# Performance work log

Hardware: AMD Instinct MI355X
Metric: run time of the kernel (lower is better)

## Reference

```python
import jax, jax.numpy as jnp
import numpy as np

EMB = 256  # embedding_dim


def setup_inputs() -> dict:
    key = jax.random.key(0)
    k1, k2, k3 = jax.random.split(key, 3)
    B, P, N, D = 32, 4, 1024, EMB
    x = jax.random.normal(k1, (B, P, N, D), dtype=jnp.float32)
    W_qkv = jax.random.normal(k2, (D, 1 + 2 * D), dtype=jnp.float32) * (1.0 / np.sqrt(D))
    b_qkv = jnp.zeros((1 + 2 * D,), dtype=jnp.float32)
    W_o = jax.random.normal(k3, (D, D), dtype=jnp.float32) * (1.0 / np.sqrt(D))
    b_o = jnp.zeros((D,), dtype=jnp.float32)
    return {"x": x, "W_qkv": W_qkv, "b_qkv": b_qkv, "W_o": W_o, "b_o": b_o}


def reference(x, W_qkv, b_qkv, W_o, b_o):
    # x: [B, P, N, D]
    D = W_o.shape[0]
    qkv = jnp.einsum('bpnd,de->bpne', x, W_qkv) + b_qkv  # [B,P,N,1+2D]
    q = qkv[..., :1]                 # [B,P,N,1]
    k = qkv[..., 1:1 + D]            # [B,P,N,D]
    v = jax.nn.relu(qkv[..., 1 + D:])  # [B,P,N,D]
    # softmax over the patch axis N (axis=2)
    context_scores = jax.nn.softmax(q, axis=2)  # [B,P,N,1]
    # dropout layers operate in inference mode here (identity)
    context_vector = jnp.sum(k * context_scores, axis=2, keepdims=True)  # [B,P,1,D]
    updated_values = v * context_vector  # broadcast multiply, [B,P,N,D]
    final = jnp.einsum('bpnd,de->bpne', updated_values, W_o) + b_o  # [B,P,N,D]
    return final
```

## Files before the change

### kernel.cpp

```cpp
#include <hip/hip_runtime.h>


typedef float  floatx4 __attribute__((ext_vector_type(4)));
typedef __bf16 bf16x8  __attribute__((ext_vector_type(8)));
typedef unsigned short u16;
typedef u16 u16x8 __attribute__((ext_vector_type(8)));

#define NGRP 128

__device__ __forceinline__ float bf2f(u16 u) {
    union { unsigned int i; float f; } c; c.i = ((unsigned int)u) << 16; return c.f;
}
__device__ __forceinline__ u16 f2bf(float f) {
    union { __bf16 h; u16 u; } c; c.h = (__bf16)f; return c.u;
}
__device__ __forceinline__ floatx4 mfma16(bf16x8 a, bf16x8 b, floatx4 c) {
    return __builtin_amdgcn_mfma_f32_16x16x32_bf16(a, b, c, 0, 0, 0);
}

__global__ __launch_bounds__(256, 4) void k_sum(
    const float* __restrict__ x, const float* __restrict__ Wqkv,
    const float* __restrict__ Wo, const float* __restrict__ bqkv,
    float* __restrict__ y, float* __restrict__ Sg,
    u16* __restrict__ Wvp, u16* __restrict__ Wop)
{
    const int tid = threadIdx.x;
    const int m0 = blockIdx.x * 64;
    const int g  = blockIdx.x >> 4;
    const int cc = tid & 31, r0 = tid >> 5;
    const int w = tid >> 6, lane = tid & 63;
    __shared__ float e_s[64];
    __shared__ float ws4[4 * 256];

    if (blockIdx.x < 256) {
        const int i = blockIdx.x * 256 + tid;
        const int j = i & 7, pl = (i >> 3) & 63, kk = (i >> 9) & 7, ct = i >> 12;
        const int k = kk * 32 + (pl >> 4) * 8 + j;
        Wvp[i] = f2bf(Wqkv[k * 513 + (257 + ct * 16 + (pl & 15))]);
        Wop[i] = f2bf(Wo[k * 256 + (ct * 16 + (pl & 15))]);
    }

    float wqv[8];
    {
        const float* wb = Wqkv + (size_t)(cc * 8) * 513;
#pragma unroll
        for (int j = 0; j < 8; ++j) wqv[j] = wb[(size_t)j * 513];
    }

    float qp[8];
    u16x8 o[8];
#pragma unroll
    for (int i = 0; i < 8; ++i) {
        const int row = r0 + 8 * i;
        const float* xp = x + (size_t)(m0 + row) * 256 + cc * 8;
        floatx4 u0 = *(const floatx4*)xp;
        floatx4 u1 = *(const floatx4*)(xp + 4);
        qp[i] = u0[0] * wqv[0] + u0[1] * wqv[1] + u0[2] * wqv[2] + u0[3] * wqv[3]
              + u1[0] * wqv[4] + u1[1] * wqv[5] + u1[2] * wqv[6] + u1[3] * wqv[7];
        u16x8 t;
        t[0] = f2bf(u0[0]); t[1] = f2bf(u0[1]); t[2] = f2bf(u0[2]); t[3] = f2bf(u0[3]);
        t[4] = f2bf(u1[0]); t[5] = f2bf(u1[1]); t[6] = f2bf(u1[2]); t[7] = f2bf(u1[3]);
        o[i] = t;
    }

#pragma unroll
    for (int m = 1; m <= 16; m <<= 1) {
#pragma unroll
        for (int i = 0; i < 8; ++i) qp[i] += __shfl_xor(qp[i], m, 64);
    }
    if ((tid & 31) == 0) {
        const float bq0 = bqkv[0];
#pragma unroll
        for (int i = 0; i < 8; ++i) e_s[r0 + 8 * i] = __expf(qp[i] + bq0);
    }
    __syncthreads();

    float yacc[8];
#pragma unroll
    for (int j = 0; j < 8; ++j) yacc[j] = 0.f;
#pragma unroll
    for (int i = 0; i < 8; ++i) {
        const float e = e_s[r0 + 8 * i];
#pragma unroll
        for (int j = 0; j < 8; ++j) yacc[j] += e * bf2f(o[i][j]);
    }
#pragma unroll
    for (int j = 0; j < 8; ++j) yacc[j] += __shfl_xor(yacc[j], 32, 64);
    if (lane < 32) {
#pragma unroll
        for (int j = 0; j < 8; ++j) ws4[w * 256 + lane * 8 + j] = yacc[j];
    }
    __syncthreads();

    if (tid < 64) {
        float e = e_s[tid];
#pragma unroll
        for (int s = 32; s > 0; s >>= 1) e += __shfl_xor(e, s, 64);
        if (tid == 0) atomicAdd(Sg + g, e);
    }
    {
        const float s = ws4[tid] + ws4[256 + tid] + ws4[512 + tid] + ws4[768 + tid];
        atomicAdd(y + g * 256 + tid, s);
    }
}

__global__ __launch_bounds__(256) void k_cv(
    const float* __restrict__ Wqkv, const float* __restrict__ bqkv,
    const float* __restrict__ y, const float* __restrict__ Sg,
    float* __restrict__ cv)
{
    const int g = blockIdx.x, d = threadIdx.x;
    __shared__ float ys[256];
    ys[d] = y[g * 256 + d] * (1.0f / Sg[g]);
    __syncthreads();
    float acc = bqkv[1 + d];
    const float* wp = Wqkv + 1 + d;
#pragma unroll 4
    for (int t = 0; t < 256; t++) acc += ys[t] * wp[(size_t)t * 513];
    cv[g * 256 + d] = acc;
}

__global__ __launch_bounds__(256, 4) void k_vo(
    const float* __restrict__ x, const u16* __restrict__ Wvp,
    const u16* __restrict__ Wop, const float* __restrict__ cv,
    const float* __restrict__ bqkv, const float* __restrict__ bo,
    float* __restrict__ out)
{
    const int tid = threadIdx.x;
    const int w = tid >> 6, lane = tid & 63, quad = lane >> 4, n16 = lane & 15;
    const int m0 = blockIdx.x * 64;
    const int g  = blockIdx.x >> 4;
    const int cc = tid & 31, r0 = tid >> 5;

    __shared__ u16 As[64 * 256];
    __shared__ float cvs[256];

    cvs[tid] = cv[g * 256 + tid];

#pragma unroll
    for (int i = 0; i < 8; ++i) {
        const int row = r0 + 8 * i;
        const float* xp = x + (size_t)(m0 + row) * 256 + cc * 8;
        floatx4 u0 = *(const floatx4*)xp;
        floatx4 u1 = *(const floatx4*)(xp + 4);
        u16x8 t;
        t[0] = f2bf(u0[0]); t[1] = f2bf(u0[1]); t[2] = f2bf(u0[2]); t[3] = f2bf(u0[3]);
        t[4] = f2bf(u1[0]); t[5] = f2bf(u1[1]); t[6] = f2bf(u1[2]); t[7] = f2bf(u1[3]);
        *(u16x8*)(As + row * 256 + ((cc ^ (row & 15)) * 8)) = t;
    }
    __syncthreads();

    floatx4 acc[4][4];
#pragma unroll
    for (int i = 0; i < 4; i++)
#pragma unroll
        for (int rt = 0; rt < 4; rt++) acc[i][rt] = (floatx4){0.f, 0.f, 0.f, 0.f};
#pragma unroll
    for (int kk = 0; kk < 8; kk++) {
        bf16x8 a[4];
#pragma unroll
        for (int rt = 0; rt < 4; rt++) {
            const int row = rt * 16 + n16;
            a[rt] = __builtin_bit_cast(bf16x8,
                *(const u16x8*)(&As[row * 256 + (((kk * 4 + quad) ^ n16) * 8)]));
        }
#pragma unroll
        for (int i = 0; i < 4; i++) {
            const int ct = w + 4 * i;
            bf16x8 bfr = __builtin_bit_cast(bf16x8,
                *(const u16x8*)(Wvp + (size_t)((ct * 8 + kk) * 64 + lane) * 8));
#pragma unroll
            for (int rt = 0; rt < 4; rt++) acc[i][rt] = mfma16(a[rt], bfr, acc[i][rt]);
        }
    }
    __syncthreads();

#pragma unroll
    for (int i = 0; i < 4; i++) {
        const int col = (w + 4 * i) * 16 + n16;
        const float bias = bqkv[257 + col];
        const float scale = cvs[col];
        const int cchunk = col >> 3, co = col & 7;
#pragma unroll
        for (int rt = 0; rt < 4; rt++) {
#pragma unroll
            for (int r = 0; r < 4; r++) {
                const int row = rt * 16 + quad * 4 + r;
                As[row * 256 + ((cchunk ^ (row & 15)) * 8) + co] =
                    f2bf(fmaxf(acc[i][rt][r] + bias, 0.f) * scale);
            }
        }
    }
    __syncthreads();

    floatx4 acc2[4][4];
#pragma unroll
    for (int i = 0; i < 4; i++)
#pragma unroll
        for (int rt = 0; rt < 4; rt++) acc2[i][rt] = (floatx4){0.f, 0.f, 0.f, 0.f};
#pragma unroll
    for (int kk = 0; kk < 8; kk++) {
        bf16x8 a[4];
#pragma unroll
        for (int rt = 0; rt < 4; rt++) {
            const int row = rt * 16 + n16;
            a[rt] = __builtin_bit_cast(bf16x8,
                *(const u16x8*)(&As[row * 256 + (((kk * 4 + quad) ^ n16) * 8)]));
        }
#pragma unroll
        for (int i = 0; i < 4; i++) {
            const int ct = w + 4 * i;
            bf16x8 bfr = __builtin_bit_cast(bf16x8,
                *(const u16x8*)(Wop + (size_t)((ct * 8 + kk) * 64 + lane) * 8));
#pragma unroll
            for (int rt = 0; rt < 4; rt++) acc2[i][rt] = mfma16(a[rt], bfr, acc2[i][rt]);
        }
    }

#pragma unroll
    for (int i = 0; i < 4; i++) {
        const int col = (w + 4 * i) * 16 + n16;
        const float bias = bo[col];
#pragma unroll
        for (int rt = 0; rt < 4; rt++) {
            const int rowb = m0 + rt * 16 + quad * 4;
#pragma unroll
            for (int r = 0; r < 4; r++)
                out[(size_t)(rowb + r) * 256 + col] = acc2[i][rt][r] + bias;
        }
    }
}

extern "C" void kernel_launch(void* const* d_in, const int* in_sizes, int n_in,
                              void* d_out, int out_size, void* d_ws, size_t ws_size,
                              hipStream_t stream)
{
    const float* x    = (const float*)d_in[0];
    const float* Wqkv = (const float*)d_in[1];
    const float* bqkv = (const float*)d_in[2];
    const float* Wo   = (const float*)d_in[3];
    const float* bo   = (const float*)d_in[4];
    float* out = (float*)d_out;

    char* ws = (char*)d_ws;
    u16*   Wvp = (u16*)(ws);
    u16*   Wop = (u16*)(ws + 131072);
    float* cv  = (float*)(ws + 262144);
    float* y   = (float*)(ws + 393216);
    float* Sg  = (float*)(ws + 524288);

    hipMemsetAsync(ws + 393216, 0, 131584, stream);
    k_sum<<<2048, 256, 0, stream>>>(x, Wqkv, Wo, bqkv, y, Sg, Wvp, Wop);
    k_cv <<<NGRP, 256, 0, stream>>>(Wqkv, bqkv, y, Sg, cv);
    k_vo <<<2048, 256, 0, stream>>>(x, Wvp, Wop, cv, bqkv, bo, out);
}
```

Before: 339.7 us.

## Cache bf16 copy of x in k_sum, load via LDS DMA in k_vo

The first pass now writes a pre-swizzled bf16 copy of x to workspace, so the second kernel reads half the bytes and copies it straight into LDS with global_load_lds instead of re-reading fp32 x and converting it. k_vo is restructured so each wave owns 16 rows and all 16 column tiles, which removes block-level syncthreads. k_sum is reorganized into 128-row blocks with a butterfly reduction for q. The cost is an extra 64MB bf16 write in k_sum and per-wave reloads of the weight fragments from global memory.

```diff
diff --git a/kernel.cpp b/kernel.cpp
--- a/kernel.cpp
+++ b/kernel.cpp
@@ -5,6 +5,7 @@
 typedef __bf16 bf16x8  __attribute__((ext_vector_type(8)));
 typedef unsigned short u16;
 typedef u16 u16x8 __attribute__((ext_vector_type(8)));
+typedef u16 u16x4 __attribute__((ext_vector_type(4)));
 
 #define NGRP 128
 
@@ -16,92 +17,105 @@
 }
 __device__ __forceinline__ floatx4 mfma16(bf16x8 a, bf16x8 b, floatx4 c) {
     return __builtin_amdgcn_mfma_f32_16x16x32_bf16(a, b, c, 0, 0, 0);
+}
+
+__device__ __forceinline__ void dma16(const u16* src, u16* lds) {
+    __builtin_amdgcn_global_load_lds(
+        (const __attribute__((address_space(1))) unsigned int*)src,
+        (__attribute__((address_space(3))) unsigned int*)lds, 16, 0, 0);
 }
 
 __global__ __launch_bounds__(256, 4) void k_sum(
     const float* __restrict__ x, const float* __restrict__ Wqkv,
     const float* __restrict__ Wo, const float* __restrict__ bqkv,
     float* __restrict__ y, float* __restrict__ Sg,
-    u16* __restrict__ Wvp, u16* __restrict__ Wop)
+    u16* __restrict__ xb, u16* __restrict__ Wvp, u16* __restrict__ Wop)
 {
     const int tid = threadIdx.x;
-    const int m0 = blockIdx.x * 64;
-    const int g  = blockIdx.x >> 4;
-    const int cc = tid & 31, r0 = tid >> 5;
     const int w = tid >> 6, lane = tid & 63;
-    __shared__ float e_s[64];
-    __shared__ float ws4[4 * 256];
-
-    if (blockIdx.x < 256) {
-        const int i = blockIdx.x * 256 + tid;
+    const int b = blockIdx.x;
+    const int g = b >> 3;
+
+    __shared__ float e_s[4][16];
+
+    if (b < 256) {
+        const int i = b * 256 + tid;
         const int j = i & 7, pl = (i >> 3) & 63, kk = (i >> 9) & 7, ct = i >> 12;
         const int k = kk * 32 + (pl >> 4) * 8 + j;
         Wvp[i] = f2bf(Wqkv[k * 513 + (257 + ct * 16 + (pl & 15))]);
         Wop[i] = f2bf(Wo[k * 256 + (ct * 16 + (pl & 15))]);
     }
 
-    float wqv[8];
-    {
-        const float* wb = Wqkv + (size_t)(cc * 8) * 513;
-#pragma unroll
-        for (int j = 0; j < 8; ++j) wqv[j] = wb[(size_t)j * 513];
-    }
-
-    float qp[8];
-    u16x8 o[8];
-#pragma unroll
-    for (int i = 0; i < 8; ++i) {
-        const int row = r0 + 8 * i;
-        const float* xp = x + (size_t)(m0 + row) * 256 + cc * 8;
-        floatx4 u0 = *(const floatx4*)xp;
-        floatx4 u1 = *(const floatx4*)(xp + 4);
-        qp[i] = u0[0] * wqv[0] + u0[1] * wqv[1] + u0[2] * wqv[2] + u0[3] * wqv[3]
-              + u1[0] * wqv[4] + u1[1] * wqv[5] + u1[2] * wqv[6] + u1[3] * wqv[7];
-        u16x8 t;
-        t[0] = f2bf(u0[0]); t[1] = f2bf(u0[1]); t[2] = f2bf(u0[2]); t[3] = f2bf(u0[3]);
-        t[4] = f2bf(u1[0]); t[5] = f2bf(u1[1]); t[6] = f2bf(u1[2]); t[7] = f2bf(u1[3]);
-        o[i] = t;
-    }
-
-#pragma unroll
-    for (int m = 1; m <= 16; m <<= 1) {
-#pragma unroll
-        for (int i = 0; i < 8; ++i) qp[i] += __shfl_xor(qp[i], m, 64);
-    }
-    if ((tid & 31) == 0) {
-        const float bq0 = bqkv[0];
-#pragma unroll
-        for (int i = 0; i < 8; ++i) e_s[r0 + 8 * i] = __expf(qp[i] + bq0);
-    }
-    __syncthreads();
-
-    float yacc[8];
-#pragma unroll
-    for (int j = 0; j < 8; ++j) yacc[j] = 0.f;
-#pragma unroll
-    for (int i = 0; i < 8; ++i) {
-        const float e = e_s[r0 + 8 * i];
-#pragma unroll
-        for (int j = 0; j < 8; ++j) yacc[j] += e * bf2f(o[i][j]);
-    }
-#pragma unroll
-    for (int j = 0; j < 8; ++j) yacc[j] += __shfl_xor(yacc[j], 32, 64);
-    if (lane < 32) {
-#pragma unroll
-        for (int j = 0; j < 8; ++j) ws4[w * 256 + lane * 8 + j] = yacc[j];
-    }
-    __syncthreads();
-
-    if (tid < 64) {
-        float e = e_s[tid];
-#pragma unroll
-        for (int s = 32; s > 0; s >>= 1) e += __shfl_xor(e, s, 64);
-        if (tid == 0) atomicAdd(Sg + g, e);
-    }
-    {
-        const float s = ws4[tid] + ws4[256 + tid] + ws4[512 + tid] + ws4[768 + tid];
-        atomicAdd(y + g * 256 + tid, s);
-    }
+    const float bq0 = bqkv[0];
+
+    float wqv[4];
+#pragma unroll
+    for (int c = 0; c < 4; ++c) wqv[c] = Wqkv[(size_t)(lane * 4 + c) * 513];
+
+    float yacc[4] = {0.f, 0.f, 0.f, 0.f};
+    float Sacc = 0.f;
+
+#pragma unroll
+    for (int s = 0; s < 2; ++s) {
+        const int m0 = b * 128 + w * 16 + s * 64;
+        u16* xt = xb + (size_t)(b * 8 + w + s * 4) * 4096;
+
+        float p[16];
+        u16x4 o[16];
+#pragma unroll
+        for (int r = 0; r < 16; ++r) {
+            floatx4 u = *(const floatx4*)(x + (size_t)(m0 + r) * 256 + lane * 4);
+            p[r] = u[0] * wqv[0] + u[1] * wqv[1] + u[2] * wqv[2] + u[3] * wqv[3];
+            u16x4 h;
+            h[0] = f2bf(u[0]); h[1] = f2bf(u[1]); h[2] = f2bf(u[2]); h[3] = f2bf(u[3]);
+            o[r] = h;
+            *(u16x4*)(xt + r * 256 + (((lane >> 1) ^ r) * 8 + (lane & 1) * 4)) = h;
+        }
+
+        float t8[8];
+#pragma unroll
+        for (int i = 0; i < 8; ++i) {
+            const float a = p[2 * i], c = p[2 * i + 1];
+            t8[i] = ((lane & 1) ? c : a) + __shfl_xor((lane & 1) ? a : c, 1, 64);
+        }
+        float t4[4];
+#pragma unroll
+        for (int i = 0; i < 4; ++i) {
+            const float a = t8[2 * i], c = t8[2 * i + 1];
+            t4[i] = ((lane & 2) ? c : a) + __shfl_xor((lane & 2) ? a : c, 2, 64);
+        }
+        float t2[2];
+#pragma unroll
+        for (int i = 0; i < 2; ++i) {
+            const float a = t4[2 * i], c = t4[2 * i + 1];
+            t2[i] = ((lane & 4) ? c : a) + __shfl_xor((lane & 4) ? a : c, 4, 64);
+        }
+        float q;
+        {
+            const float a = t2[0], c = t2[1];
+            q = ((lane & 8) ? c : a) + __shfl_xor((lane & 8) ? a : c, 8, 64);
+        }
+        q += __shfl_xor(q, 16, 64);
+        q += __shfl_xor(q, 32, 64);
+
+        const float e = __expf(q + bq0);
+        if (lane < 16) { e_s[w][lane] = e; Sacc += e; }
+
+#pragma unroll
+        for (int r = 0; r < 16; ++r) {
+            const float er = e_s[w][r];
+            yacc[0] += er * bf2f(o[r][0]);
+            yacc[1] += er * bf2f(o[r][1]);
+            yacc[2] += er * bf2f(o[r][2]);
+            yacc[3] += er * bf2f(o[r][3]);
+        }
+    }
+
+#pragma unroll
+    for (int m = 1; m <= 32; m <<= 1) Sacc += __shfl_xor(Sacc, m, 64);
+    if (lane == 0) atomicAdd(Sg + g, Sacc);
+#pragma unroll
+    for (int j = 0; j < 4; ++j) atomicAdd(y + g * 256 + lane * 4 + j, yacc[j]);
 }
 
 __global__ __launch_bounds__(256) void k_cv(
@@ -121,113 +135,81 @@
 }
 
 __global__ __launch_bounds__(256, 4) void k_vo(
-    const float* __restrict__ x, const u16* __restrict__ Wvp,
+    const u16* __restrict__ xb, const u16* __restrict__ Wvp,
     const u16* __restrict__ Wop, const float* __restrict__ cv,
     const float* __restrict__ bqkv, const float* __restrict__ bo,
     float* __restrict__ out)
 {
     const int tid = threadIdx.x;
-    const int w = tid >> 6, lane = tid & 63, quad = lane >> 4, n16 = lane & 15;
-    const int m0 = blockIdx.x * 64;
-    const int g  = blockIdx.x >> 4;
-    const int cc = tid & 31, r0 = tid >> 5;
-
-    __shared__ u16 As[64 * 256];
-    __shared__ float cvs[256];
-
-    cvs[tid] = cv[g * 256 + tid];
-
-#pragma unroll
-    for (int i = 0; i < 8; ++i) {
-        const int row = r0 + 8 * i;
-        const float* xp = x + (size_t)(m0 + row) * 256 + cc * 8;
-        floatx4 u0 = *(const floatx4*)xp;
-        floatx4 u1 = *(const floatx4*)(xp + 4);
-        u16x8 t;
-        t[0] = f2bf(u0[0]); t[1] = f2bf(u0[1]); t[2] = f2bf(u0[2]); t[3] = f2bf(u0[3]);
-        t[4] = f2bf(u1[0]); t[5] = f2bf(u1[1]); t[6] = f2bf(u1[2]); t[7] = f2bf(u1[3]);
-        *(u16x8*)(As + row * 256 + ((cc ^ (row & 15)) * 8)) = t;
-    }
-    __syncthreads();
-
-    floatx4 acc[4][4];
-#pragma unroll
-    for (int i = 0; i < 4; i++)
-#pragma unroll
-        for (int rt = 0; rt < 4; rt++) acc[i][rt] = (floatx4){0.f, 0.f, 0.f, 0.f};
-#pragma unroll
-    for (int kk = 0; kk < 8; kk++) {
-        bf16x8 a[4];
-#pragma unroll
-        for (int rt = 0; rt < 4; rt++) {
-            const int row = rt * 16 + n16;
-            a[rt] = __builtin_bit_cast(bf16x8,
-                *(const u16x8*)(&As[row * 256 + (((kk * 4 + quad) ^ n16) * 8)]));
-        }
-#pragma unroll
-        for (int i = 0; i < 4; i++) {
-            const int ct = w + 4 * i;
+    const int w = tid >> 6, lane = tid & 63;
+    const int quad = lane >> 4, n16 = lane & 15;
+    const int j = blockIdx.x * 4 + w;
+    const int m0 = j * 16;
+    const int g  = j >> 6;
+
+    __shared__ u16 As[4][4096];
+    u16* S = As[w];
+
+    {
+        const u16* src = xb + (size_t)j * 4096;
+#pragma unroll
+        for (int i = 0; i < 8; ++i)
+            dma16(src + i * 512 + lane * 8, S + i * 512);
+    }
+    __builtin_amdgcn_sched_barrier(0);
+    asm volatile("s_waitcnt vmcnt(0)" ::: "memory");
+    __builtin_amdgcn_sched_barrier(0);
+
+    floatx4 acc[16];
+#pragma unroll
+    for (int ct = 0; ct < 16; ++ct) acc[ct] = (floatx4){0.f, 0.f, 0.f, 0.f};
+#pragma unroll
+    for (int kk = 0; kk < 8; ++kk) {
+        bf16x8 a = __builtin_bit_cast(bf16x8,
+            *(const u16x8*)(S + n16 * 256 + (((kk * 4 + quad) ^ n16) * 8)));
+#pragma unroll
+        for (int ct = 0; ct < 16; ++ct) {
             bf16x8 bfr = __builtin_bit_cast(bf16x8,
                 *(const u16x8*)(Wvp + (size_t)((ct * 8 + kk) * 64 + lane) * 8));
-#pragma unroll
-            for (int rt = 0; rt < 4; rt++) acc[i][rt] = mfma16(a[rt], bfr, acc[i][rt]);
-        }
-    }
-    __syncthreads();
-
-#pragma unroll
-    for (int i = 0; i < 4; i++) {
-        const int col = (w + 4 * i) * 16 + n16;
-        const float bias = bqkv[257 + col];
-        const float scale = cvs[col];
-        const int cchunk = col >> 3, co = col & 7;
-#pragma unroll
-        for (int rt = 0; rt < 4; rt++) {
-#pragma unroll
-            for (int r = 0; r < 4; r++) {
-                const int row = rt * 16 + quad * 4 + r;
-                As[row * 256 + ((cchunk ^ (row & 15)) * 8) + co] =
-                    f2bf(fmaxf(acc[i][rt][r] + bias, 0.f) * scale);
-            }
-        }
-    }
-    __syncthreads();
-
-    floatx4 acc2[4][4];
-#pragma unroll
-    for (int i = 0; i < 4; i++)
-#pragma unroll
-        for (int rt = 0; rt < 4; rt++) acc2[i][rt] = (floatx4){0.f, 0.f, 0.f, 0.f};
-#pragma unroll
-    for (int kk = 0; kk < 8; kk++) {
-        bf16x8 a[4];
-#pragma unroll
-        for (int rt = 0; rt < 4; rt++) {
-            const int row = rt * 16 + n16;
-            a[rt] = __builtin_bit_cast(bf16x8,
-                *(const u16x8*)(&As[row * 256 + (((kk * 4 + quad) ^ n16) * 8)]));
-        }
-#pragma unroll
-        for (int i = 0; i < 4; i++) {
-            const int ct = w + 4 * i;
+            acc[ct] = mfma16(a, bfr, acc[ct]);
+        }
+    }
+
+#pragma unroll
+    for (int ct = 0; ct < 16; ++ct) {
+        const int col = ct * 16 + n16;
+        const float bv = bqkv[257 + col];
+        const float cvv = cv[g * 256 + col];
+#pragma unroll
+        for (int r = 0; r < 4; ++r) {
+            const int row = quad * 4 + r;
+            S[row * 256 + ((((col >> 3) ^ row) * 8) + (col & 7))] =
+                f2bf(fmaxf(acc[ct][r] + bv, 0.f) * cvv);
+        }
+    }
+
+    floatx4 acc2[16];
+#pragma unroll
+    for (int ct = 0; ct < 16; ++ct) acc2[ct] = (floatx4){0.f, 0.f, 0.f, 0.f};
+#pragma unroll
+    for (int kk = 0; kk < 8; ++kk) {
+        bf16x8 a = __builtin_bit_cast(bf16x8,
+            *(const u16x8*)(S + n16 * 256 + (((kk * 4 + quad) ^ n16) * 8)));
+#pragma unroll
+        for (int ct = 0; ct < 16; ++ct) {
             bf16x8 bfr = __builtin_bit_cast(bf16x8,
                 *(const u16x8*)(Wop + (size_t)((ct * 8 + kk) * 64 + lane) * 8));
-#pragma unroll
-            for (int rt = 0; rt < 4; rt++) acc2[i][rt] = mfma16(a[rt], bfr, acc2[i][rt]);
-        }
-    }
-
-#pragma unroll
-    for (int i = 0; i < 4; i++) {
-        const int col = (w + 4 * i) * 16 + n16;
-        const float bias = bo[col];
-#pragma unroll
-        for (int rt = 0; rt < 4; rt++) {
-            const int rowb = m0 + rt * 16 + quad * 4;
-#pragma unroll
-            for (int r = 0; r < 4; r++)
-                out[(size_t)(rowb + r) * 256 + col] = acc2[i][rt][r] + bias;
-        }
+            acc2[ct] = mfma16(a, bfr, acc2[ct]);
+        }
+    }
+
+#pragma unroll
+    for (int ct = 0; ct < 16; ++ct) {
+        const int col = ct * 16 + n16;
+        const float bb = bo[col];
+#pragma unroll
+        for (int r = 0; r < 4; ++r)
+            out[(size_t)(m0 + quad * 4 + r) * 256 + col] = acc2[ct][r] + bb;
     }
 }
 
@@ -248,9 +230,10 @@
     float* cv  = (float*)(ws + 262144);
     float* y   = (float*)(ws + 393216);
     float* Sg  = (float*)(ws + 524288);
+    u16*   xb  = (u16*)(ws + 524800);
 
     hipMemsetAsync(ws + 393216, 0, 131584, stream);
-    k_sum<<<2048, 256, 0, stream>>>(x, Wqkv, Wo, bqkv, y, Sg, Wvp, Wop);
+    k_sum<<<1024, 256, 0, stream>>>(x, Wqkv, Wo, bqkv, y, Sg, xb, Wvp, Wop);
     k_cv <<<NGRP, 256, 0, stream>>>(Wqkv, bqkv, y, Sg, cv);
-    k_vo <<<2048, 256, 0, stream>>>(x, Wvp, Wop, cv, bqkv, bo, out);
-}
+    k_vo <<<2048, 256, 0, stream>>>(xb, Wvp, Wop, cv, bqkv, bo, out);
+}
```

Result: slower. 496.7 us (+46.2%).
